# Optimization experiments

Hardware: AMD Instinct MI355X
Metric: run time of the kernel (lower is better)

## Reference

```python
import jax, jax.numpy as jnp
import numpy as np

MAX_SHIFT = 15
EPS = 1e-8


def setup_inputs() -> dict:
    key = jax.random.key(0)
    k1, k2 = jax.random.split(key)
    B, T = 2048, 2048
    preds = jax.random.normal(k1, (B, T), dtype=jnp.float32)
    targets = jax.random.normal(k2, (B, T), dtype=jnp.float32)
    return {"preds": preds, "targets": targets}


def reference(preds, targets):
    # targets statistics (shared across shifts)
    tc = targets - jnp.mean(targets, axis=1, keepdims=True)          # [B, T]
    std_t = jnp.sqrt(jnp.sum(tc * tc, axis=1) + EPS)                 # [B]

    shifts = jnp.arange(-MAX_SHIFT, MAX_SHIFT + 1)                   # [S]

    def pearson_for_shift(s):
        ps = jnp.roll(preds, s, axis=1)                              # [B, T]
        pc = ps - jnp.mean(ps, axis=1, keepdims=True)
        std_p = jnp.sqrt(jnp.sum(pc * pc, axis=1) + EPS)             # [B]
        cov = jnp.sum(pc * tc, axis=1)                               # [B]
        return cov / (std_p * std_t)

    pearsons = jax.vmap(pearson_for_shift)(shifts)                   # [S, B]
    best = jnp.maximum(jnp.max(pearsons, axis=0), -1.0)              # [B], init -1
    return 1.0 - jnp.mean(best)
```

## Files before the change

kernel.cpp:

```cpp
#include <hip/hip_runtime.h>

#define TLEN 2048
#define BROWS 2048
#define NSHIFT 31
#define MAXSH 15
#define BLOCK 256
#define EPSF 1e-8f

__device__ __forceinline__ int padidx(int k) { return k + ((k >> 3) << 1); }

__global__ void __launch_bounds__(BLOCK, 4)
pearson_rows_kernel(const float* __restrict__ preds,
                    const float* __restrict__ targets,
                    float* __restrict__ row_best)
{
    __shared__ float smem[NSHIFT * BLOCK + 20];
    float* rbuf = smem + NSHIFT * BLOCK;
    float* wmax = rbuf + 16;

    const int tid  = threadIdx.x;
    const int wave = tid >> 6;
    const int lane = tid & 63;
    const int row  = blockIdx.x;
    const float* p_row = preds   + (size_t)row * TLEN;
    const float* t_row = targets + (size_t)row * TLEN;

    float pc[8];
    {
        float4 a = ((const float4*)p_row)[2 * tid];
        float4 b = ((const float4*)p_row)[2 * tid + 1];
        pc[0] = a.x; pc[1] = a.y; pc[2] = a.z; pc[3] = a.w;
        pc[4] = b.x; pc[5] = b.y; pc[6] = b.z; pc[7] = b.w;
    }
    float sp = 0.f, spp = 0.f;
    #pragma unroll
    for (int i = 0; i < 8; ++i) { sp += pc[i]; spp = fmaf(pc[i], pc[i], spp); }

    float st = 0.f, stt = 0.f;
    #pragma unroll
    for (int r = 0; r < 2; ++r) {
        int f4 = tid + r * BLOCK;
        float4 tv = ((const float4*)t_row)[f4];
        st  += tv.x + tv.y + tv.z + tv.w;
        stt = fmaf(tv.x, tv.x, stt); stt = fmaf(tv.y, tv.y, stt);
        stt = fmaf(tv.z, tv.z, stt); stt = fmaf(tv.w, tv.w, stt);
        int k = f4 * 4 + MAXSH;
        smem[padidx(k)]     = tv.x;
        smem[padidx(k + 1)] = tv.y;
        smem[padidx(k + 2)] = tv.z;
        smem[padidx(k + 3)] = tv.w;
    }
    if (tid < MAXSH) {
        smem[padidx(tid)] = t_row[TLEN - MAXSH + tid];
    } else if (tid >= 32 && tid < 32 + MAXSH) {
        int i = tid - 32;
        smem[padidx(TLEN + MAXSH + i)] = t_row[i];
    }

    #pragma unroll
    for (int off = 32; off > 0; off >>= 1) {
        sp  += __shfl_xor(sp,  off);
        spp += __shfl_xor(spp, off);
        st  += __shfl_xor(st,  off);
        stt += __shfl_xor(stt, off);
    }
    if (lane == 0) {
        rbuf[wave * 4 + 0] = sp;  rbuf[wave * 4 + 1] = spp;
        rbuf[wave * 4 + 2] = st;  rbuf[wave * 4 + 3] = stt;
    }
    __syncthreads();

    float w[38];
    {
        const int base = 10 * tid;
        #pragma unroll
        for (int q = 0; q < 19; ++q) {
            int d = 2 * q;
            float2 v = *(const float2*)(smem + base + d + 2 * (d >> 3));
            w[d]     = v.x;
            w[d + 1] = v.y;
        }
        #pragma unroll
        for (int d = 0; d < 38; ++d) {
            asm volatile("" : "+v"(w[d]));
        }
    }
    __syncthreads();

    float acc[NSHIFT];
    #pragma unroll
    for (int s = 0; s < NSHIFT; ++s) acc[s] = 0.f;
    #pragma unroll
    for (int m = 0; m < 8; ++m) {
        #pragma unroll
        for (int s = 0; s < NSHIFT; ++s) acc[s] = fmaf(pc[m], w[m + s], acc[s]);
    }

    #pragma unroll
    for (int s = 0; s < NSHIFT; ++s) smem[s * BLOCK + tid] = acc[s];
    __syncthreads();

    float dmax = -1e30f;
    const int s0 = wave * 8;
    const int s1 = (s0 + 8 < NSHIFT) ? s0 + 8 : NSHIFT;
    for (int s = s0; s < s1; ++s) {
        float v = smem[s * BLOCK + lane]       + smem[s * BLOCK + lane + 64]
                + smem[s * BLOCK + lane + 128] + smem[s * BLOCK + lane + 192];
        #pragma unroll
        for (int off = 32; off > 0; off >>= 1) v += __shfl_xor(v, off);
        dmax = fmaxf(dmax, v);
    }
    if (lane == 0) wmax[wave] = dmax;
    __syncthreads();

    if (tid == 0) {
        float dot = fmaxf(fmaxf(wmax[0], wmax[1]), fmaxf(wmax[2], wmax[3]));
        float SP = 0, SPP = 0, ST = 0, STT = 0;
        #pragma unroll
        for (int w2 = 0; w2 < 4; ++w2) {
            SP += rbuf[w2 * 4 + 0]; SPP += rbuf[w2 * 4 + 1];
            ST += rbuf[w2 * 4 + 2]; STT += rbuf[w2 * 4 + 3];
        }
        const float invT = 1.0f / TLEN;
        float mp = SP * invT, mt = ST * invT;
        float varp = SPP - (float)TLEN * mp * mp;
        float vart = STT - (float)TLEN * mt * mt;
        float corr = (float)TLEN * mp * mt;
        float pear = (dot - corr) * rsqrtf((varp + EPSF) * (vart + EPSF));
        row_best[row] = fmaxf(pear, -1.0f);
    }
}

__global__ void __launch_bounds__(BLOCK)
pearson_finalize_kernel(const float* __restrict__ row_best, float* __restrict__ out)
{
    __shared__ float r[4];
    const int tid = threadIdx.x, wave = tid >> 6, lane = tid & 63;
    float4 a = ((const float4*)row_best)[tid];
    float4 b = ((const float4*)row_best)[tid + BLOCK];
    float s = (a.x + a.y) + (a.z + a.w) + (b.x + b.y) + (b.z + b.w);
    #pragma unroll
    for (int off = 32; off > 0; off >>= 1) s += __shfl_xor(s, off);
    if (lane == 0) r[wave] = s;
    __syncthreads();
    if (tid == 0)
        out[0] = 1.0f - (r[0] + r[1] + r[2] + r[3]) * (1.0f / (float)BROWS);
}

extern "C" void kernel_launch(void* const* d_in, const int* in_sizes, int n_in,
                              void* d_out, int out_size, void* d_ws, size_t ws_size,
                              hipStream_t stream) {
    const float* preds   = (const float*)d_in[0];
    const float* targets = (const float*)d_in[1];
    float* row_best = (float*)d_ws;
    float* out      = (float*)d_out;
    pearson_rows_kernel<<<BROWS, BLOCK, 0, stream>>>(preds, targets, row_best);
    pearson_finalize_kernel<<<1, BLOCK, 0, stream>>>(row_best, out);
}
```

Baseline: 85.70 us.

## Use DPP wave reductions, shrink shared memory, and drop a block barrier

Replaces shuffle-based reductions with DPP row/broadcast reductions. Each wave now reduces all 31 shift accumulators in registers and writes only per-wave partials, instead of staging a 31x256 array in shared memory. This shrinks LDS from about 31 KB to about 13 KB, which can allow more resident blocks per CU, and removes one __syncthreads. The target window now uses a 12-stride padded layout so it can be read with float4 loads. The cost is 31 DPP reduction chains per thread and some correctness risk in the DPP control/mask choices and the reduce-to-lane-63 assumption.

```diff
diff --git a/kernel.cpp b/kernel.cpp
--- a/kernel.cpp
+++ b/kernel.cpp
@@ -7,16 +7,40 @@
 #define BLOCK 256
 #define EPSF 1e-8f
 
-__device__ __forceinline__ int padidx(int k) { return k + ((k >> 3) << 1); }
+__device__ __forceinline__ int padidx12(int k) { return 12 * (k >> 3) + (k & 7); }
+
+template<int CTRL, int RMASK, bool BC>
+__device__ __forceinline__ float dpp_mov(float v, float old) {
+    return __int_as_float(__builtin_amdgcn_update_dpp(
+        __float_as_int(old), __float_as_int(v), CTRL, RMASK, 0xF, BC));
+}
+__device__ __forceinline__ float wave_sum_dpp(float v) {
+    v += dpp_mov<0x111, 0xF, true>(v, 0.f);
+    v += dpp_mov<0x112, 0xF, true>(v, 0.f);
+    v += dpp_mov<0x114, 0xF, true>(v, 0.f);
+    v += dpp_mov<0x118, 0xF, true>(v, 0.f);
+    v += dpp_mov<0x142, 0xA, true>(v, 0.f);
+    v += dpp_mov<0x143, 0xC, true>(v, 0.f);
+    return v;
+}
+__device__ __forceinline__ float wave_max_dpp(float v) {
+    v = fmaxf(v, dpp_mov<0x111, 0xF, false>(v, v));
+    v = fmaxf(v, dpp_mov<0x112, 0xF, false>(v, v));
+    v = fmaxf(v, dpp_mov<0x114, 0xF, false>(v, v));
+    v = fmaxf(v, dpp_mov<0x118, 0xF, false>(v, v));
+    v = fmaxf(v, dpp_mov<0x142, 0xA, false>(v, v));
+    v = fmaxf(v, dpp_mov<0x143, 0xC, false>(v, v));
+    return v;
+}
 
 __global__ void __launch_bounds__(BLOCK, 4)
 pearson_rows_kernel(const float* __restrict__ preds,
                     const float* __restrict__ targets,
                     float* __restrict__ row_best)
 {
-    __shared__ float smem[NSHIFT * BLOCK + 20];
-    float* rbuf = smem + NSHIFT * BLOCK;
-    float* wmax = rbuf + 16;
+    __shared__ float smem[3392];
+    float* wsum = smem + 3120;
+    float* rbuf = smem + 3376;
 
     const int tid  = threadIdx.x;
     const int wave = tid >> 6;
@@ -45,47 +69,44 @@
         stt = fmaf(tv.x, tv.x, stt); stt = fmaf(tv.y, tv.y, stt);
         stt = fmaf(tv.z, tv.z, stt); stt = fmaf(tv.w, tv.w, stt);
         int k = f4 * 4 + MAXSH;
-        smem[padidx(k)]     = tv.x;
-        smem[padidx(k + 1)] = tv.y;
-        smem[padidx(k + 2)] = tv.z;
-        smem[padidx(k + 3)] = tv.w;
+        smem[padidx12(k)]     = tv.x;
+        smem[padidx12(k + 1)] = tv.y;
+        smem[padidx12(k + 2)] = tv.z;
+        smem[padidx12(k + 3)] = tv.w;
     }
     if (tid < MAXSH) {
-        smem[padidx(tid)] = t_row[TLEN - MAXSH + tid];
+        smem[padidx12(tid)] = t_row[TLEN - MAXSH + tid];
     } else if (tid >= 32 && tid < 32 + MAXSH) {
         int i = tid - 32;
-        smem[padidx(TLEN + MAXSH + i)] = t_row[i];
+        smem[padidx12(TLEN + MAXSH + i)] = t_row[i];
     }
 
-    #pragma unroll
-    for (int off = 32; off > 0; off >>= 1) {
-        sp  += __shfl_xor(sp,  off);
-        spp += __shfl_xor(spp, off);
-        st  += __shfl_xor(st,  off);
-        stt += __shfl_xor(stt, off);
-    }
-    if (lane == 0) {
-        rbuf[wave * 4 + 0] = sp;  rbuf[wave * 4 + 1] = spp;
-        rbuf[wave * 4 + 2] = st;  rbuf[wave * 4 + 3] = stt;
+    sp  = wave_sum_dpp(sp);
+    spp = wave_sum_dpp(spp);
+    st  = wave_sum_dpp(st);
+    stt = wave_sum_dpp(stt);
+    if (lane == 63) {
+        *(float4*)(rbuf + wave * 4) = make_float4(sp, spp, st, stt);
     }
     __syncthreads();
 
     float w[38];
     {
-        const int base = 10 * tid;
+        const float* g = smem + 12 * tid;
         #pragma unroll
-        for (int q = 0; q < 19; ++q) {
-            int d = 2 * q;
-            float2 v = *(const float2*)(smem + base + d + 2 * (d >> 3));
-            w[d]     = v.x;
-            w[d + 1] = v.y;
+        for (int q = 0; q < 4; ++q) {
+            float4 a = *(const float4*)(g + 12 * q);
+            float4 b = *(const float4*)(g + 12 * q + 4);
+            w[8*q + 0] = a.x; w[8*q + 1] = a.y; w[8*q + 2] = a.z; w[8*q + 3] = a.w;
+            w[8*q + 4] = b.x; w[8*q + 5] = b.y; w[8*q + 6] = b.z; w[8*q + 7] = b.w;
         }
+        float4 c = *(const float4*)(g + 48);
+        float2 e = *(const float2*)(g + 52);
+        w[32] = c.x; w[33] = c.y; w[34] = c.z; w[35] = c.w;
+        w[36] = e.x; w[37] = e.y;
         #pragma unroll
-        for (int d = 0; d < 38; ++d) {
-            asm volatile("" : "+v"(w[d]));
-        }
+        for (int d = 0; d < 38; ++d) asm volatile("" : "+v"(w[d]));
     }
-    __syncthreads();
 
     float acc[NSHIFT];
     #pragma unroll
@@ -97,37 +118,40 @@
     }
 
     #pragma unroll
-    for (int s = 0; s < NSHIFT; ++s) smem[s * BLOCK + tid] = acc[s];
+    for (int s = 0; s < NSHIFT; ++s) acc[s] = wave_sum_dpp(acc[s]);
+    if (lane == 63) {
+        float* dst = wsum + wave * 64;
+        *(float4*)(dst +  0) = make_float4(acc[0],  acc[1],  acc[2],  acc[3]);
+        *(float4*)(dst +  4) = make_float4(acc[4],  acc[5],  acc[6],  acc[7]);
+        *(float4*)(dst +  8) = make_float4(acc[8],  acc[9],  acc[10], acc[11]);
+        *(float4*)(dst + 12) = make_float4(acc[12], acc[13], acc[14], acc[15]);
+        *(float4*)(dst + 16) = make_float4(acc[16], acc[17], acc[18], acc[19]);
+        *(float4*)(dst + 20) = make_float4(acc[20], acc[21], acc[22], acc[23]);
+        *(float4*)(dst + 24) = make_float4(acc[24], acc[25], acc[26], acc[27]);
+        *(float2*)(dst + 28) = make_float2(acc[28], acc[29]);
+        dst[30] = acc[30];
+    }
     __syncthreads();
 
-    float dmax = -1e30f;
-    const int s0 = wave * 8;
-    const int s1 = (s0 + 8 < NSHIFT) ? s0 + 8 : NSHIFT;
-    for (int s = s0; s < s1; ++s) {
-        float v = smem[s * BLOCK + lane]       + smem[s * BLOCK + lane + 64]
-                + smem[s * BLOCK + lane + 128] + smem[s * BLOCK + lane + 192];
-        #pragma unroll
-        for (int off = 32; off > 0; off >>= 1) v += __shfl_xor(v, off);
-        dmax = fmaxf(dmax, v);
-    }
-    if (lane == 0) wmax[wave] = dmax;
-    __syncthreads();
-
-    if (tid == 0) {
-        float dot = fmaxf(fmaxf(wmax[0], wmax[1]), fmaxf(wmax[2], wmax[3]));
-        float SP = 0, SPP = 0, ST = 0, STT = 0;
-        #pragma unroll
-        for (int w2 = 0; w2 < 4; ++w2) {
-            SP += rbuf[w2 * 4 + 0]; SPP += rbuf[w2 * 4 + 1];
-            ST += rbuf[w2 * 4 + 2]; STT += rbuf[w2 * 4 + 3];
-        }
+    if (wave == 0) {
+        float dot = wsum[lane] + wsum[64 + lane] + wsum[128 + lane] + wsum[192 + lane];
+        float4 r0 = *(const float4*)(rbuf + 0);
+        float4 r1 = *(const float4*)(rbuf + 4);
+        float4 r2 = *(const float4*)(rbuf + 8);
+        float4 r3 = *(const float4*)(rbuf + 12);
+        float SP  = r0.x + r1.x + r2.x + r3.x;
+        float SPP = r0.y + r1.y + r2.y + r3.y;
+        float ST  = r0.z + r1.z + r2.z + r3.z;
+        float STT = r0.w + r1.w + r2.w + r3.w;
         const float invT = 1.0f / TLEN;
         float mp = SP * invT, mt = ST * invT;
         float varp = SPP - (float)TLEN * mp * mp;
         float vart = STT - (float)TLEN * mt * mt;
         float corr = (float)TLEN * mp * mt;
         float pear = (dot - corr) * rsqrtf((varp + EPSF) * (vart + EPSF));
-        row_best[row] = fmaxf(pear, -1.0f);
+        float v = (lane < NSHIFT) ? pear : -3.0e38f;
+        v = wave_max_dpp(v);
+        if (lane == 63) row_best[row] = fmaxf(v, -1.0f);
     }
 }
 
@@ -139,9 +163,8 @@
     float4 a = ((const float4*)row_best)[tid];
     float4 b = ((const float4*)row_best)[tid + BLOCK];
     float s = (a.x + a.y) + (a.z + a.w) + (b.x + b.y) + (b.z + b.w);
-    #pragma unroll
-    for (int off = 32; off > 0; off >>= 1) s += __shfl_xor(s, off);
-    if (lane == 0) r[wave] = s;
+    s = wave_sum_dpp(s);
+    if (lane == 63) r[wave] = s;
     __syncthreads();
     if (tid == 0)
         out[0] = 1.0f - (r[0] + r[1] + r[2] + r[3]) * (1.0f / (float)BROWS);
```

Result: faster. 80.90 us (-5.6%).
